# Kernel optimization log

Hardware: AMD Instinct MI355X
Metric: run time of the kernel (lower is better)

## Reference

```python
import jax, jax.numpy as jnp
import numpy as np

N, B, CIN = 2048, 16, 1
M = 4096
COUT = 64
R = 128


def setup_inputs() -> dict:
    key = jax.random.key(0)
    k1, k2, k3, k4, k5 = jax.random.split(key, 5)
    return {
        "context_in": jax.random.normal(k1, (N, B, CIN), dtype=jnp.float32),
        "context_out": jax.random.normal(k2, (N, B, COUT), dtype=jnp.float32),
        "target_in": jax.random.normal(k3, (M, B, CIN), dtype=jnp.float32),
        "lengthscale": jnp.ones((1,), dtype=jnp.float32),
        "W": jax.random.normal(k4, (R, COUT + 1), dtype=jnp.float32),
        "b": jax.random.normal(k5, (R,), dtype=jnp.float32),
    }


def reference(context_in, context_out, target_in, lengthscale, W, b):
    # context_in: (N,B,Cin), context_out: (N,B,Cout), target_in: (M,B,Cin)
    n, batch, _ = context_in.shape
    # density channel prepended -> (N,B,Cout+1)
    dens = jnp.ones((n, batch, 1), dtype=context_in.dtype)
    co = jnp.concatenate([dens, context_out], axis=-1)
    ci = jnp.transpose(context_in, (1, 0, 2))   # (B,N,Cin)
    ti = jnp.transpose(target_in, (1, 0, 2))    # (B,M,Cin)
    # squared pairwise distances (B,N,M)
    d2 = (jnp.sum(ci * ci, -1)[:, :, None]
          + jnp.sum(ti * ti, -1)[:, None, :]
          - 2.0 * jnp.einsum('bnd,bmd->bnm', ci, ti))
    d2 = jnp.maximum(d2, 0.0)
    # RBF kernel: exp(-0.5 * d2 / lengthscale^2)
    K = jnp.exp(-0.5 * d2 / (lengthscale[0] ** 2))  # (B,N,M)
    # weighted sum over context points: (B,M,Cout+1)
    out = jnp.einsum('nbc,bnm->bmc', co, K)
    # density normalization of non-density channels
    out = jnp.concatenate([out[..., :1], out[..., 1:] / (out[..., :1] + 1e-8)], axis=-1)
    # linear projection (Cout+1 -> R)
    out = out @ W.T + b
    return jnp.transpose(out, (1, 0, 2))  # (M,B,R)
```

## Files before the change

### kernel.cpp

```cpp
#include <hip/hip_runtime.h>
#include <hip/hip_bf16.h>


#define N_CTX 2048
#define BATCH 16
#define M_TGT 4096
#define COUT  64
#define RDIM  128

#define WS_CO_BYTES (N_CTX * BATCH * COUT * 2)
#define WS_SX_OFF   WS_CO_BYTES
#define WS_WT_OFF   (WS_SX_OFF + N_CTX * BATCH * 4)

#define SSCALE 0.8493222f

typedef __attribute__((ext_vector_type(8)))  short        bf16x8;
typedef __attribute__((ext_vector_type(4)))  float        floatx4;
typedef __attribute__((ext_vector_type(4)))  unsigned int uint4v;

#if __has_builtin(__builtin_amdgcn_exp2f)
#define EXP2F __builtin_amdgcn_exp2f
#else
#define EXP2F exp2f
#endif

static __device__ __forceinline__ unsigned int pack_bf16(float lo, float hi) {
    __hip_bfloat162 h = __float22bfloat162_rn(make_float2(lo, hi));
    return *reinterpret_cast<unsigned int*>(&h);
}
static __device__ __forceinline__ unsigned short f2bf(float f) {
    __hip_bfloat16 h = __float2bfloat16(f);
    return *reinterpret_cast<unsigned short*>(&h);
}

__global__ __launch_bounds__(256)
void convdeepset_prep(const float* __restrict__ ci, const float* __restrict__ co,
                      const float* __restrict__ ls, const float* __restrict__ W,
                      unsigned char* __restrict__ ws)
{
    unsigned short* cow = (unsigned short*)ws;
    float*          sx  = (float*)(ws + WS_SX_OFF);
    unsigned short* wt  = (unsigned short*)(ws + WS_WT_OFF);
    const int blk = blockIdx.x, tid = threadIdx.x;

    if (blk < 1024) {
        const int g    = blk * 4 + (tid >> 6);
        const int bb   = g & 15;
        const int nblk = g >> 4;
        const int c    = tid & 63;
        const float* rp = co + ((size_t)nblk * 8 * BATCH + bb) * COUT + c;
        unsigned int u[4];
#pragma unroll
        for (int j = 0; j < 4; ++j) {
            const float f0 = rp[(size_t)(2 * j)     * BATCH * COUT];
            const float f1 = rp[(size_t)(2 * j + 1) * BATCH * COUT];
            u[j] = pack_bf16(f0, f1);
        }
        *(uint4v*)&cow[(size_t)bb * 131072 + nblk * 512 + c * 8] = *(uint4v*)u;
    } else if (blk < 1152) {
        const int f = (blk - 1024) * 256 + tid;
        const int n = f & 2047, bb = f >> 11;
        const float s = SSCALE / ls[0];
        sx[bb * 2048 + n] = s * ci[(size_t)n * BATCH + bb];
    } else {
        for (int f = tid; f < 8192; f += 256) {
            const int cp = f & 7, r = (f >> 3) & 127, ch = f >> 10;
            wt[ch * 1024 + r * 8 + cp] = f2bf(W[r * 65 + 1 + ch * 8 + cp]);
        }
    }
}

__global__ __launch_bounds__(256)
void convdeepset_main(const float* __restrict__ ti, const float* __restrict__ ls,
                      const float* __restrict__ W,  const float* __restrict__ bias,
                      const unsigned char* __restrict__ ws, float* __restrict__ out)
{
    __shared__ float sxt[N_CTX];
    __shared__ unsigned short slab[2][8192];
    __shared__ unsigned short vstage[4][2][1024];
    __shared__ float w0l[RDIM], biasl[RDIM];

    const int tid  = threadIdx.x;
    const int lane = tid & 63;
    const int wv   = tid >> 6;
    const int g2   = lane >> 4;
    const int l15  = lane & 15;

    const int xcd = blockIdx.x & 7;
    const int i   = blockIdx.x >> 3;
    const int b   = xcd * 2 + (i & 1);
    const int mt  = i >> 1;
    const int m0  = mt * 128 + wv * 32;

    const float4* sxg = (const float4*)(ws + WS_SX_OFF) + b * (N_CTX / 4);
    ((float4*)sxt)[tid]       = sxg[tid];
    ((float4*)sxt)[tid + 256] = sxg[tid + 256];
    if (tid < RDIM) { w0l[tid] = W[tid * 65]; biasl[tid] = bias[tid]; }

    const float s   = SSCALE / ls[0];
    const float sy0 = s * ti[(size_t)(m0 + l15) * BATCH + b];
    const float sy1 = s * ti[(size_t)(m0 + 16 + l15) * BATCH + b];

    const unsigned short* cowb = (const unsigned short*)ws + (size_t)b * 131072;

    typedef const __attribute__((address_space(1))) unsigned int* gp_t;
    typedef __attribute__((address_space(3))) unsigned int* lp_t;
    auto stage = [&](int period, int buf) {
        const unsigned short* gsrc = cowb + (size_t)period * 8192;
#pragma unroll
        for (int j = 0; j < 4; ++j) {
            const int ch = wv * 4 + j;
            __builtin_amdgcn_global_load_lds((gp_t)(gsrc + ch * 512 + lane * 8),
                                             (lp_t)(&slab[buf][ch * 512]),
                                             16, 0, 0);
        }
    };

    const short onebf = (short)0x3F80;
    bf16x8 ones;
#pragma unroll
    for (int j = 0; j < 8; ++j) ones[j] = onebf;

    floatx4 acc0[4], acc1[4], accd0, accd1;
#pragma unroll
    for (int q = 0; q < 4; ++q)
#pragma unroll
        for (int e = 0; e < 4; ++e) { acc0[q][e] = 0.0f; acc1[q][e] = 0.0f; }
#pragma unroll
    for (int e = 0; e < 4; ++e) { accd0[e] = 0.0f; accd1[e] = 0.0f; }

    stage(0, 0);
    __syncthreads();

    for (int p = 0; p < 16; ++p) {
        if (p + 1 < 16) stage(p + 1, (p + 1) & 1);
        const unsigned short* sb = &slab[p & 1][0];
#pragma unroll
        for (int k2 = 0; k2 < 4; ++k2) {
            const int ks = p * 4 + k2;
            const float* xp = &sxt[ks * 32 + g2 * 8];
            const float4 xa = *(const float4*)(xp);
            const float4 xb = *(const float4*)(xp + 4);
            const unsigned short* bp = sb + (k2 * 4 + g2) * 512 + l15 * 8;
            const bf16x8 c0 = *(const bf16x8*)(bp);
            const bf16x8 c1 = *(const bf16x8*)(bp + 128);
            const bf16x8 c2 = *(const bf16x8*)(bp + 256);
            const bf16x8 c3 = *(const bf16x8*)(bp + 384);
            const float xs[8] = {xa.x, xa.y, xa.z, xa.w, xb.x, xb.y, xb.z, xb.w};
            float kv0[8], kv1[8];
#pragma unroll
            for (int j = 0; j < 8; ++j) {
                float t0 = xs[j] - sy0; kv0[j] = EXP2F(-(t0 * t0));
                float t1 = xs[j] - sy1; kv1[j] = EXP2F(-(t1 * t1));
            }
            uint4v aw0, aw1;
#pragma unroll
            for (int q = 0; q < 4; ++q) {
                aw0[q] = pack_bf16(kv0[2 * q], kv0[2 * q + 1]);
                aw1[q] = pack_bf16(kv1[2 * q], kv1[2 * q + 1]);
            }
            const bf16x8 av0 = __builtin_bit_cast(bf16x8, aw0);
            const bf16x8 av1 = __builtin_bit_cast(bf16x8, aw1);
            acc0[0] = __builtin_amdgcn_mfma_f32_16x16x32_bf16(av0, c0, acc0[0], 0, 0, 0);
            acc0[1] = __builtin_amdgcn_mfma_f32_16x16x32_bf16(av0, c1, acc0[1], 0, 0, 0);
            acc0[2] = __builtin_amdgcn_mfma_f32_16x16x32_bf16(av0, c2, acc0[2], 0, 0, 0);
            acc0[3] = __builtin_amdgcn_mfma_f32_16x16x32_bf16(av0, c3, acc0[3], 0, 0, 0);
            accd0   = __builtin_amdgcn_mfma_f32_16x16x32_bf16(av0, ones, accd0, 0, 0, 0);
            acc1[0] = __builtin_amdgcn_mfma_f32_16x16x32_bf16(av1, c0, acc1[0], 0, 0, 0);
            acc1[1] = __builtin_amdgcn_mfma_f32_16x16x32_bf16(av1, c1, acc1[1], 0, 0, 0);
            acc1[2] = __builtin_amdgcn_mfma_f32_16x16x32_bf16(av1, c2, acc1[2], 0, 0, 0);
            acc1[3] = __builtin_amdgcn_mfma_f32_16x16x32_bf16(av1, c3, acc1[3], 0, 0, 0);
            accd1   = __builtin_amdgcn_mfma_f32_16x16x32_bf16(av1, ones, accd1, 0, 0, 0);
        }
        __syncthreads();
    }

    const unsigned short* wtg = (const unsigned short*)(ws + WS_WT_OFF);
#pragma unroll
    for (int tile = 0; tile < 2; ++tile) {
        const floatx4* acc  = tile ? acc1 : acc0;
        const floatx4  accd = tile ? accd1 : accd0;
        float drow[4], dinv[4];
#pragma unroll
        for (int e = 0; e < 4; ++e) {
            drow[e] = accd[e];
            dinv[e] = 1.0f / (accd[e] + 1e-8f);
        }
        unsigned short* vs = vstage[wv][tile];
#pragma unroll
        for (int reg = 0; reg < 4; ++reg) {
            const int m = (lane >> 4) * 4 + reg;
#pragma unroll
            for (int q = 0; q < 4; ++q) {
                const int c = q * 16 + l15;
                vs[(c >> 3) * 128 + m * 8 + (c & 7)] = f2bf(acc[q][reg]);
            }
        }
        floatx4 pacc[8];
#pragma unroll
        for (int rt = 0; rt < 8; ++rt)
#pragma unroll
            for (int e = 0; e < 4; ++e) pacc[rt][e] = 0.0f;
#pragma unroll
        for (int s2 = 0; s2 < 2; ++s2) {
            const int ch = s2 * 4 + g2;
            const bf16x8 avp = *(const bf16x8*)&vs[ch * 128 + l15 * 8];
#pragma unroll
            for (int rt = 0; rt < 8; ++rt) {
                const bf16x8 bvp = *(const bf16x8*)&wtg[ch * 1024 + (rt * 16 + l15) * 8];
                pacc[rt] = __builtin_amdgcn_mfma_f32_16x16x32_bf16(avp, bvp, pacc[rt], 0, 0, 0);
            }
        }
#pragma unroll
        for (int rt = 0; rt < 8; ++rt) {
            const int r = rt * 16 + l15;
            const float w0v = w0l[r];
            const float bv  = biasl[r];
#pragma unroll
            for (int reg = 0; reg < 4; ++reg) {
                const int m = (lane >> 4) * 4 + reg;
                out[((size_t)(m0 + tile * 16 + m) * BATCH + b) * RDIM + r]
                    = pacc[rt][reg] * dinv[reg] + drow[reg] * w0v + bv;
            }
        }
    }
}

extern "C" void kernel_launch(void* const* d_in, const int* in_sizes, int n_in,
                              void* d_out, int out_size, void* d_ws, size_t ws_size,
                              hipStream_t stream) {
    const float* ci   = (const float*)d_in[0];
    const float* co   = (const float*)d_in[1];
    const float* ti   = (const float*)d_in[2];
    const float* ls   = (const float*)d_in[3];
    const float* W    = (const float*)d_in[4];
    const float* bias = (const float*)d_in[5];
    float* o = (float*)d_out;
    (void)in_sizes; (void)n_in; (void)out_size; (void)ws_size;

    convdeepset_prep<<<1153, 256, 0, stream>>>(ci, co, ls, W, (unsigned char*)d_ws);
    convdeepset_main<<<512, 256, 0, stream>>>(
        ti, ls, W, bias, (const unsigned char*)d_ws, o);
}
```

Baseline: 121.9 us.

## Factor RBF exponent into FMA form and use 512-thread blocks

The exponent -(x-y)^2 is rewritten as 2xy - x^2 with the -y^2 factor applied once in the epilogue (exp(-y^2) scales both density and channel sums, so normalization cancels it). The per-element kernel cost drops from sub, mul, neg to a single FMA before exp2. Blocks are doubled to 512 threads, with each wave owning one 16-row target tile instead of two, halving accumulator registers and raising wave count. Risk: numerical range of exp2(2xy - x^2) can overflow or underflow differently than the original for large |y|, and the density output row is reconstructed by multiplication.

```diff
diff --git a/kernel.cpp b/kernel.cpp
--- a/kernel.cpp
+++ b/kernel.cpp
@@ -9,8 +9,9 @@
 #define RDIM  128
 
 #define WS_CO_BYTES (N_CTX * BATCH * COUT * 2)
-#define WS_SX_OFF   WS_CO_BYTES
-#define WS_WT_OFF   (WS_SX_OFF + N_CTX * BATCH * 4)
+#define WS_SXA_OFF  WS_CO_BYTES
+#define WS_SXB_OFF  (WS_SXA_OFF + N_CTX * BATCH * 4)
+#define WS_WT_OFF   (WS_SXB_OFF + N_CTX * BATCH * 4)
 
 #define SSCALE 0.8493222f
 
@@ -39,7 +40,8 @@
                       unsigned char* __restrict__ ws)
 {
     unsigned short* cow = (unsigned short*)ws;
-    float*          sx  = (float*)(ws + WS_SX_OFF);
+    float*          sxa = (float*)(ws + WS_SXA_OFF);
+    float*          sxb = (float*)(ws + WS_SXB_OFF);
     unsigned short* wt  = (unsigned short*)(ws + WS_WT_OFF);
     const int blk = blockIdx.x, tid = threadIdx.x;
 
@@ -61,7 +63,9 @@
         const int f = (blk - 1024) * 256 + tid;
         const int n = f & 2047, bb = f >> 11;
         const float s = SSCALE / ls[0];
-        sx[bb * 2048 + n] = s * ci[(size_t)n * BATCH + bb];
+        const float v = s * ci[(size_t)n * BATCH + bb];
+        sxa[bb * 2048 + n] = v + v;
+        sxb[bb * 2048 + n] = -v * v;
     } else {
         for (int f = tid; f < 8192; f += 256) {
             const int cp = f & 7, r = (f >> 3) & 127, ch = f >> 10;
@@ -70,15 +74,17 @@
     }
 }
 
-__global__ __launch_bounds__(256)
+__global__ __launch_bounds__(512, 4)
 void convdeepset_main(const float* __restrict__ ti, const float* __restrict__ ls,
                       const float* __restrict__ W,  const float* __restrict__ bias,
                       const unsigned char* __restrict__ ws, float* __restrict__ out)
 {
-    __shared__ float sxt[N_CTX];
+    __shared__ float sxa[N_CTX];
+    __shared__ float sxb[N_CTX];
     __shared__ unsigned short slab[2][8192];
-    __shared__ unsigned short vstage[4][2][1024];
+    __shared__ unsigned short vstage[8][1024];
     __shared__ float w0l[RDIM], biasl[RDIM];
+    __shared__ float syt[128];
 
     const int tid  = threadIdx.x;
     const int lane = tid & 63;
@@ -90,16 +96,17 @@
     const int i   = blockIdx.x >> 3;
     const int b   = xcd * 2 + (i & 1);
     const int mt  = i >> 1;
-    const int m0  = mt * 128 + wv * 32;
-
-    const float4* sxg = (const float4*)(ws + WS_SX_OFF) + b * (N_CTX / 4);
-    ((float4*)sxt)[tid]       = sxg[tid];
-    ((float4*)sxt)[tid + 256] = sxg[tid + 256];
+    const int m0  = mt * 128 + wv * 16;
+
+    const float4* sag = (const float4*)(ws + WS_SXA_OFF) + b * (N_CTX / 4);
+    const float4* sbg = (const float4*)(ws + WS_SXB_OFF) + b * (N_CTX / 4);
+    ((float4*)sxa)[tid] = sag[tid];
+    ((float4*)sxb)[tid] = sbg[tid];
     if (tid < RDIM) { w0l[tid] = W[tid * 65]; biasl[tid] = bias[tid]; }
 
-    const float s   = SSCALE / ls[0];
-    const float sy0 = s * ti[(size_t)(m0 + l15) * BATCH + b];
-    const float sy1 = s * ti[(size_t)(m0 + 16 + l15) * BATCH + b];
+    const float s  = SSCALE / ls[0];
+    const float sy = s * ti[(size_t)(m0 + l15) * BATCH + b];
+    if (g2 == 0) syt[wv * 16 + l15] = sy * sy;
 
     const unsigned short* cowb = (const unsigned short*)ws + (size_t)b * 131072;
 
@@ -108,8 +115,8 @@
     auto stage = [&](int period, int buf) {
         const unsigned short* gsrc = cowb + (size_t)period * 8192;
 #pragma unroll
-        for (int j = 0; j < 4; ++j) {
-            const int ch = wv * 4 + j;
+        for (int j = 0; j < 2; ++j) {
+            const int ch = wv * 2 + j;
             __builtin_amdgcn_global_load_lds((gp_t)(gsrc + ch * 512 + lane * 8),
                                              (lp_t)(&slab[buf][ch * 512]),
                                              16, 0, 0);
@@ -121,13 +128,13 @@
 #pragma unroll
     for (int j = 0; j < 8; ++j) ones[j] = onebf;
 
-    floatx4 acc0[4], acc1[4], accd0, accd1;
+    floatx4 acc[4], accd;
 #pragma unroll
     for (int q = 0; q < 4; ++q)
 #pragma unroll
-        for (int e = 0; e < 4; ++e) { acc0[q][e] = 0.0f; acc1[q][e] = 0.0f; }
-#pragma unroll
-    for (int e = 0; e < 4; ++e) { accd0[e] = 0.0f; accd1[e] = 0.0f; }
+        for (int e = 0; e < 4; ++e) acc[q][e] = 0.0f;
+#pragma unroll
+    for (int e = 0; e < 4; ++e) accd[e] = 0.0f;
 
     stage(0, 0);
     __syncthreads();
@@ -138,90 +145,80 @@
 #pragma unroll
         for (int k2 = 0; k2 < 4; ++k2) {
             const int ks = p * 4 + k2;
-            const float* xp = &sxt[ks * 32 + g2 * 8];
-            const float4 xa = *(const float4*)(xp);
-            const float4 xb = *(const float4*)(xp + 4);
+            const float* xap = &sxa[ks * 32 + g2 * 8];
+            const float* xbp = &sxb[ks * 32 + g2 * 8];
+            const floatx4 arg0 = (*(const floatx4*)xap)       * sy + (*(const floatx4*)xbp);
+            const floatx4 arg1 = (*(const floatx4*)(xap + 4)) * sy + (*(const floatx4*)(xbp + 4));
             const unsigned short* bp = sb + (k2 * 4 + g2) * 512 + l15 * 8;
             const bf16x8 c0 = *(const bf16x8*)(bp);
             const bf16x8 c1 = *(const bf16x8*)(bp + 128);
             const bf16x8 c2 = *(const bf16x8*)(bp + 256);
             const bf16x8 c3 = *(const bf16x8*)(bp + 384);
-            const float xs[8] = {xa.x, xa.y, xa.z, xa.w, xb.x, xb.y, xb.z, xb.w};
-            float kv0[8], kv1[8];
-#pragma unroll
-            for (int j = 0; j < 8; ++j) {
-                float t0 = xs[j] - sy0; kv0[j] = EXP2F(-(t0 * t0));
-                float t1 = xs[j] - sy1; kv1[j] = EXP2F(-(t1 * t1));
-            }
-            uint4v aw0, aw1;
-#pragma unroll
-            for (int q = 0; q < 4; ++q) {
-                aw0[q] = pack_bf16(kv0[2 * q], kv0[2 * q + 1]);
-                aw1[q] = pack_bf16(kv1[2 * q], kv1[2 * q + 1]);
-            }
-            const bf16x8 av0 = __builtin_bit_cast(bf16x8, aw0);
-            const bf16x8 av1 = __builtin_bit_cast(bf16x8, aw1);
-            acc0[0] = __builtin_amdgcn_mfma_f32_16x16x32_bf16(av0, c0, acc0[0], 0, 0, 0);
-            acc0[1] = __builtin_amdgcn_mfma_f32_16x16x32_bf16(av0, c1, acc0[1], 0, 0, 0);
-            acc0[2] = __builtin_amdgcn_mfma_f32_16x16x32_bf16(av0, c2, acc0[2], 0, 0, 0);
-            acc0[3] = __builtin_amdgcn_mfma_f32_16x16x32_bf16(av0, c3, acc0[3], 0, 0, 0);
-            accd0   = __builtin_amdgcn_mfma_f32_16x16x32_bf16(av0, ones, accd0, 0, 0, 0);
-            acc1[0] = __builtin_amdgcn_mfma_f32_16x16x32_bf16(av1, c0, acc1[0], 0, 0, 0);
-            acc1[1] = __builtin_amdgcn_mfma_f32_16x16x32_bf16(av1, c1, acc1[1], 0, 0, 0);
-            acc1[2] = __builtin_amdgcn_mfma_f32_16x16x32_bf16(av1, c2, acc1[2], 0, 0, 0);
-            acc1[3] = __builtin_amdgcn_mfma_f32_16x16x32_bf16(av1, c3, acc1[3], 0, 0, 0);
-            accd1   = __builtin_amdgcn_mfma_f32_16x16x32_bf16(av1, ones, accd1, 0, 0, 0);
+            float kv[8];
+            kv[0] = EXP2F(arg0.x); kv[1] = EXP2F(arg0.y);
+            kv[2] = EXP2F(arg0.z); kv[3] = EXP2F(arg0.w);
+            kv[4] = EXP2F(arg1.x); kv[5] = EXP2F(arg1.y);
+            kv[6] = EXP2F(arg1.z); kv[7] = EXP2F(arg1.w);
+            uint4v aw;
+#pragma unroll
+            for (int q = 0; q < 4; ++q)
+                aw[q] = pack_bf16(kv[2 * q], kv[2 * q + 1]);
+            const bf16x8 av = __builtin_bit_cast(bf16x8, aw);
+            acc[0] = __builtin_amdgcn_mfma_f32_16x16x32_bf16(av, c0, acc[0], 0, 0, 0);
+            acc[1] = __builtin_amdgcn_mfma_f32_16x16x32_bf16(av, c1, acc[1], 0, 0, 0);
+            acc[2] = __builtin_amdgcn_mfma_f32_16x16x32_bf16(av, c2, acc[2], 0, 0, 0);
+            acc[3] = __builtin_amdgcn_mfma_f32_16x16x32_bf16(av, c3, acc[3], 0, 0, 0);
+            accd   = __builtin_amdgcn_mfma_f32_16x16x32_bf16(av, ones, accd, 0, 0, 0);
         }
         __syncthreads();
     }
 
     const unsigned short* wtg = (const unsigned short*)(ws + WS_WT_OFF);
-#pragma unroll
-    for (int tile = 0; tile < 2; ++tile) {
-        const floatx4* acc  = tile ? acc1 : acc0;
-        const floatx4  accd = tile ? accd1 : accd0;
-        float drow[4], dinv[4];
-#pragma unroll
-        for (int e = 0; e < 4; ++e) {
-            drow[e] = accd[e];
-            dinv[e] = 1.0f / (accd[e] + 1e-8f);
-        }
-        unsigned short* vs = vstage[wv][tile];
+
+    float dt[4], ff[4];
+#pragma unroll
+    for (int reg = 0; reg < 4; ++reg) {
+        const int m  = (lane >> 4) * 4 + reg;
+        const float e = EXP2F(-syt[wv * 16 + m]);
+        dt[reg] = accd[reg] * e;
+        ff[reg] = e / (dt[reg] + 1e-8f);
+    }
+
+    unsigned short* vs = vstage[wv];
+#pragma unroll
+    for (int reg = 0; reg < 4; ++reg) {
+        const int m = (lane >> 4) * 4 + reg;
+#pragma unroll
+        for (int q = 0; q < 4; ++q) {
+            const int c = q * 16 + l15;
+            vs[(c >> 3) * 128 + m * 8 + (c & 7)] = f2bf(acc[q][reg]);
+        }
+    }
+    floatx4 pacc[8];
+#pragma unroll
+    for (int rt = 0; rt < 8; ++rt)
+#pragma unroll
+        for (int e = 0; e < 4; ++e) pacc[rt][e] = 0.0f;
+#pragma unroll
+    for (int s2 = 0; s2 < 2; ++s2) {
+        const int ch = s2 * 4 + g2;
+        const bf16x8 avp = *(const bf16x8*)&vs[ch * 128 + l15 * 8];
+#pragma unroll
+        for (int rt = 0; rt < 8; ++rt) {
+            const bf16x8 bvp = *(const bf16x8*)&wtg[ch * 1024 + (rt * 16 + l15) * 8];
+            pacc[rt] = __builtin_amdgcn_mfma_f32_16x16x32_bf16(avp, bvp, pacc[rt], 0, 0, 0);
+        }
+    }
+#pragma unroll
+    for (int rt = 0; rt < 8; ++rt) {
+        const int r = rt * 16 + l15;
+        const float w0v = w0l[r];
+        const float bv  = biasl[r];
 #pragma unroll
         for (int reg = 0; reg < 4; ++reg) {
             const int m = (lane >> 4) * 4 + reg;
-#pragma unroll
-            for (int q = 0; q < 4; ++q) {
-                const int c = q * 16 + l15;
-                vs[(c >> 3) * 128 + m * 8 + (c & 7)] = f2bf(acc[q][reg]);
-            }
-        }
-        floatx4 pacc[8];
-#pragma unroll
-        for (int rt = 0; rt < 8; ++rt)
-#pragma unroll
-            for (int e = 0; e < 4; ++e) pacc[rt][e] = 0.0f;
-#pragma unroll
-        for (int s2 = 0; s2 < 2; ++s2) {
-            const int ch = s2 * 4 + g2;
-            const bf16x8 avp = *(const bf16x8*)&vs[ch * 128 + l15 * 8];
-#pragma unroll
-            for (int rt = 0; rt < 8; ++rt) {
-                const bf16x8 bvp = *(const bf16x8*)&wtg[ch * 1024 + (rt * 16 + l15) * 8];
-                pacc[rt] = __builtin_amdgcn_mfma_f32_16x16x32_bf16(avp, bvp, pacc[rt], 0, 0, 0);
-            }
-        }
-#pragma unroll
-        for (int rt = 0; rt < 8; ++rt) {
-            const int r = rt * 16 + l15;
-            const float w0v = w0l[r];
-            const float bv  = biasl[r];
-#pragma unroll
-            for (int reg = 0; reg < 4; ++reg) {
-                const int m = (lane >> 4) * 4 + reg;
-                out[((size_t)(m0 + tile * 16 + m) * BATCH + b) * RDIM + r]
-                    = pacc[rt][reg] * dinv[reg] + drow[reg] * w0v + bv;
-            }
+            out[((size_t)(m0 + m) * BATCH + b) * RDIM + r]
+                = pacc[rt][reg] * ff[reg] + dt[reg] * w0v + bv;
         }
     }
 }
@@ -239,6 +236,6 @@
     (void)in_sizes; (void)n_in; (void)out_size; (void)ws_size;
 
     convdeepset_prep<<<1153, 256, 0, stream>>>(ci, co, ls, W, (unsigned char*)d_ws);
-    convdeepset_main<<<512, 256, 0, stream>>>(
+    convdeepset_main<<<512, 512, 0, stream>>>(
         ti, ls, W, bias, (const unsigned char*)d_ws, o);
 }
```

After: 115.8 us. 1.05x faster.

## Factor RBF exponent algebraically and stream context tiles directly from global into registers

Applied to the files above, without the earlier changes.

The exponent -(x-y)^2 is expanded into 2xy - x^2 - y^2, with 2x and -x^2 precomputed in the prep kernel, so the inner loop does one FMA per element before exp2. The per-target factor exp2(-y^2) is applied afterwards in the epilogue to both the density and the normalisation. The LDS double-buffered staging of context values and positions is replaced with a register double-buffer (two Slots) that loads directly from global memory, which removes the block barriers but raises register pressure and relies on cache reuse across waves. Pulling exp2(-y^2) out of the sum can underflow for targets far from the origin, which risks precision loss.

```diff
diff --git a/kernel.cpp b/kernel.cpp
--- a/kernel.cpp
+++ b/kernel.cpp
@@ -9,8 +9,9 @@
 #define RDIM  128
 
 #define WS_CO_BYTES (N_CTX * BATCH * COUT * 2)
-#define WS_SX_OFF   WS_CO_BYTES
-#define WS_WT_OFF   (WS_SX_OFF + N_CTX * BATCH * 4)
+#define WS_SXA_OFF  WS_CO_BYTES
+#define WS_SXB_OFF  (WS_SXA_OFF + N_CTX * BATCH * 4)
+#define WS_WT_OFF   (WS_SXB_OFF + N_CTX * BATCH * 4)
 
 #define SSCALE 0.8493222f
 
@@ -39,7 +40,8 @@
                       unsigned char* __restrict__ ws)
 {
     unsigned short* cow = (unsigned short*)ws;
-    float*          sx  = (float*)(ws + WS_SX_OFF);
+    float*          sxa = (float*)(ws + WS_SXA_OFF);
+    float*          sxb = (float*)(ws + WS_SXB_OFF);
     unsigned short* wt  = (unsigned short*)(ws + WS_WT_OFF);
     const int blk = blockIdx.x, tid = threadIdx.x;
 
@@ -61,7 +63,9 @@
         const int f = (blk - 1024) * 256 + tid;
         const int n = f & 2047, bb = f >> 11;
         const float s = SSCALE / ls[0];
-        sx[bb * 2048 + n] = s * ci[(size_t)n * BATCH + bb];
+        const float v = s * ci[(size_t)n * BATCH + bb];
+        sxa[bb * 2048 + n] = v + v;
+        sxb[bb * 2048 + n] = -v * v;
     } else {
         for (int f = tid; f < 8192; f += 256) {
             const int cp = f & 7, r = (f >> 3) & 127, ch = f >> 10;
@@ -69,16 +73,18 @@
         }
     }
 }
+
+struct Slot {
+    bf16x8  c0, c1, c2, c3;
+    floatx4 xa0, xa1, xb0, xb1;
+};
 
 __global__ __launch_bounds__(256)
 void convdeepset_main(const float* __restrict__ ti, const float* __restrict__ ls,
                       const float* __restrict__ W,  const float* __restrict__ bias,
                       const unsigned char* __restrict__ ws, float* __restrict__ out)
 {
-    __shared__ float sxt[N_CTX];
-    __shared__ unsigned short slab[2][8192];
     __shared__ unsigned short vstage[4][2][1024];
-    __shared__ float w0l[RDIM], biasl[RDIM];
 
     const int tid  = threadIdx.x;
     const int lane = tid & 63;
@@ -92,29 +98,13 @@
     const int mt  = i >> 1;
     const int m0  = mt * 128 + wv * 32;
 
-    const float4* sxg = (const float4*)(ws + WS_SX_OFF) + b * (N_CTX / 4);
-    ((float4*)sxt)[tid]       = sxg[tid];
-    ((float4*)sxt)[tid + 256] = sxg[tid + 256];
-    if (tid < RDIM) { w0l[tid] = W[tid * 65]; biasl[tid] = bias[tid]; }
-
     const float s   = SSCALE / ls[0];
     const float sy0 = s * ti[(size_t)(m0 + l15) * BATCH + b];
     const float sy1 = s * ti[(size_t)(m0 + 16 + l15) * BATCH + b];
 
     const unsigned short* cowb = (const unsigned short*)ws + (size_t)b * 131072;
-
-    typedef const __attribute__((address_space(1))) unsigned int* gp_t;
-    typedef __attribute__((address_space(3))) unsigned int* lp_t;
-    auto stage = [&](int period, int buf) {
-        const unsigned short* gsrc = cowb + (size_t)period * 8192;
-#pragma unroll
-        for (int j = 0; j < 4; ++j) {
-            const int ch = wv * 4 + j;
-            __builtin_amdgcn_global_load_lds((gp_t)(gsrc + ch * 512 + lane * 8),
-                                             (lp_t)(&slab[buf][ch * 512]),
-                                             16, 0, 0);
-        }
-    };
+    const float* sxa = (const float*)(ws + WS_SXA_OFF) + b * N_CTX;
+    const float* sxb = (const float*)(ws + WS_SXB_OFF) + b * N_CTX;
 
     const short onebf = (short)0x3F80;
     bf16x8 ones;
@@ -129,62 +119,79 @@
 #pragma unroll
     for (int e = 0; e < 4; ++e) { accd0[e] = 0.0f; accd1[e] = 0.0f; }
 
-    stage(0, 0);
-    __syncthreads();
-
-    for (int p = 0; p < 16; ++p) {
-        if (p + 1 < 16) stage(p + 1, (p + 1) & 1);
-        const unsigned short* sb = &slab[p & 1][0];
-#pragma unroll
-        for (int k2 = 0; k2 < 4; ++k2) {
-            const int ks = p * 4 + k2;
-            const float* xp = &sxt[ks * 32 + g2 * 8];
-            const float4 xa = *(const float4*)(xp);
-            const float4 xb = *(const float4*)(xp + 4);
-            const unsigned short* bp = sb + (k2 * 4 + g2) * 512 + l15 * 8;
-            const bf16x8 c0 = *(const bf16x8*)(bp);
-            const bf16x8 c1 = *(const bf16x8*)(bp + 128);
-            const bf16x8 c2 = *(const bf16x8*)(bp + 256);
-            const bf16x8 c3 = *(const bf16x8*)(bp + 384);
-            const float xs[8] = {xa.x, xa.y, xa.z, xa.w, xb.x, xb.y, xb.z, xb.w};
-            float kv0[8], kv1[8];
-#pragma unroll
-            for (int j = 0; j < 8; ++j) {
-                float t0 = xs[j] - sy0; kv0[j] = EXP2F(-(t0 * t0));
-                float t1 = xs[j] - sy1; kv1[j] = EXP2F(-(t1 * t1));
-            }
-            uint4v aw0, aw1;
-#pragma unroll
-            for (int q = 0; q < 4; ++q) {
-                aw0[q] = pack_bf16(kv0[2 * q], kv0[2 * q + 1]);
-                aw1[q] = pack_bf16(kv1[2 * q], kv1[2 * q + 1]);
-            }
-            const bf16x8 av0 = __builtin_bit_cast(bf16x8, aw0);
-            const bf16x8 av1 = __builtin_bit_cast(bf16x8, aw1);
-            acc0[0] = __builtin_amdgcn_mfma_f32_16x16x32_bf16(av0, c0, acc0[0], 0, 0, 0);
-            acc0[1] = __builtin_amdgcn_mfma_f32_16x16x32_bf16(av0, c1, acc0[1], 0, 0, 0);
-            acc0[2] = __builtin_amdgcn_mfma_f32_16x16x32_bf16(av0, c2, acc0[2], 0, 0, 0);
-            acc0[3] = __builtin_amdgcn_mfma_f32_16x16x32_bf16(av0, c3, acc0[3], 0, 0, 0);
-            accd0   = __builtin_amdgcn_mfma_f32_16x16x32_bf16(av0, ones, accd0, 0, 0, 0);
-            acc1[0] = __builtin_amdgcn_mfma_f32_16x16x32_bf16(av1, c0, acc1[0], 0, 0, 0);
-            acc1[1] = __builtin_amdgcn_mfma_f32_16x16x32_bf16(av1, c1, acc1[1], 0, 0, 0);
-            acc1[2] = __builtin_amdgcn_mfma_f32_16x16x32_bf16(av1, c2, acc1[2], 0, 0, 0);
-            acc1[3] = __builtin_amdgcn_mfma_f32_16x16x32_bf16(av1, c3, acc1[3], 0, 0, 0);
-            accd1   = __builtin_amdgcn_mfma_f32_16x16x32_bf16(av1, ones, accd1, 0, 0, 0);
-        }
-        __syncthreads();
+    auto loadk = [&](Slot& S, int k) {
+        const unsigned short* bp = cowb + ((k * 4 + g2) << 9) + l15 * 8;
+        S.c0 = *(const bf16x8*)(bp);
+        S.c1 = *(const bf16x8*)(bp + 128);
+        S.c2 = *(const bf16x8*)(bp + 256);
+        S.c3 = *(const bf16x8*)(bp + 384);
+        const float* ap  = sxa + k * 32 + g2 * 8;
+        const float* bpx = sxb + k * 32 + g2 * 8;
+        S.xa0 = *(const floatx4*)(ap);
+        S.xa1 = *(const floatx4*)(ap + 4);
+        S.xb0 = *(const floatx4*)(bpx);
+        S.xb1 = *(const floatx4*)(bpx + 4);
+    };
+
+    auto compute = [&](const Slot& S) {
+        const floatx4 a00 = S.xa0 * sy0 + S.xb0;
+        const floatx4 a01 = S.xa1 * sy0 + S.xb1;
+        const floatx4 a10 = S.xa0 * sy1 + S.xb0;
+        const floatx4 a11 = S.xa1 * sy1 + S.xb1;
+        float kv0[8], kv1[8];
+        kv0[0] = EXP2F(a00.x); kv0[1] = EXP2F(a00.y);
+        kv0[2] = EXP2F(a00.z); kv0[3] = EXP2F(a00.w);
+        kv0[4] = EXP2F(a01.x); kv0[5] = EXP2F(a01.y);
+        kv0[6] = EXP2F(a01.z); kv0[7] = EXP2F(a01.w);
+        kv1[0] = EXP2F(a10.x); kv1[1] = EXP2F(a10.y);
+        kv1[2] = EXP2F(a10.z); kv1[3] = EXP2F(a10.w);
+        kv1[4] = EXP2F(a11.x); kv1[5] = EXP2F(a11.y);
+        kv1[6] = EXP2F(a11.z); kv1[7] = EXP2F(a11.w);
+        uint4v aw0, aw1;
+#pragma unroll
+        for (int q = 0; q < 4; ++q) {
+            aw0[q] = pack_bf16(kv0[2 * q], kv0[2 * q + 1]);
+            aw1[q] = pack_bf16(kv1[2 * q], kv1[2 * q + 1]);
+        }
+        const bf16x8 av0 = __builtin_bit_cast(bf16x8, aw0);
+        const bf16x8 av1 = __builtin_bit_cast(bf16x8, aw1);
+        acc0[0] = __builtin_amdgcn_mfma_f32_16x16x32_bf16(av0, S.c0, acc0[0], 0, 0, 0);
+        acc0[1] = __builtin_amdgcn_mfma_f32_16x16x32_bf16(av0, S.c1, acc0[1], 0, 0, 0);
+        acc0[2] = __builtin_amdgcn_mfma_f32_16x16x32_bf16(av0, S.c2, acc0[2], 0, 0, 0);
+        acc0[3] = __builtin_amdgcn_mfma_f32_16x16x32_bf16(av0, S.c3, acc0[3], 0, 0, 0);
+        accd0   = __builtin_amdgcn_mfma_f32_16x16x32_bf16(av0, ones, accd0, 0, 0, 0);
+        acc1[0] = __builtin_amdgcn_mfma_f32_16x16x32_bf16(av1, S.c0, acc1[0], 0, 0, 0);
+        acc1[1] = __builtin_amdgcn_mfma_f32_16x16x32_bf16(av1, S.c1, acc1[1], 0, 0, 0);
+        acc1[2] = __builtin_amdgcn_mfma_f32_16x16x32_bf16(av1, S.c2, acc1[2], 0, 0, 0);
+        acc1[3] = __builtin_amdgcn_mfma_f32_16x16x32_bf16(av1, S.c3, acc1[3], 0, 0, 0);
+        accd1   = __builtin_amdgcn_mfma_f32_16x16x32_bf16(av1, ones, accd1, 0, 0, 0);
+    };
+
+    Slot A, B;
+    loadk(A, 0);
+    for (int p = 0; p < 64; p += 2) {
+        loadk(B, p + 1);
+        compute(A);
+        if (p + 2 < 64) loadk(A, p + 2);
+        compute(B);
     }
 
     const unsigned short* wtg = (const unsigned short*)(ws + WS_WT_OFF);
+    const float sy0sq = sy0 * sy0;
+    const float sy1sq = sy1 * sy1;
 #pragma unroll
     for (int tile = 0; tile < 2; ++tile) {
         const floatx4* acc  = tile ? acc1 : acc0;
         const floatx4  accd = tile ? accd1 : accd0;
-        float drow[4], dinv[4];
-#pragma unroll
-        for (int e = 0; e < 4; ++e) {
-            drow[e] = accd[e];
-            dinv[e] = 1.0f / (accd[e] + 1e-8f);
+        const float    sysq = tile ? sy1sq : sy0sq;
+        float dt[4], ff[4];
+#pragma unroll
+        for (int reg = 0; reg < 4; ++reg) {
+            const int m   = (lane >> 4) * 4 + reg;
+            const float ysq = __shfl(sysq, m, 64);
+            const float e   = EXP2F(-ysq);
+            dt[reg] = accd[reg] * e;
+            ff[reg] = e / (dt[reg] + 1e-8f);
         }
         unsigned short* vs = vstage[wv][tile];
 #pragma unroll
@@ -214,13 +221,13 @@
 #pragma unroll
         for (int rt = 0; rt < 8; ++rt) {
             const int r = rt * 16 + l15;
-            const float w0v = w0l[r];
-            const float bv  = biasl[r];
+            const float w0v = W[r * 65];
+            const float bv  = bias[r];
 #pragma unroll
             for (int reg = 0; reg < 4; ++reg) {
                 const int m = (lane >> 4) * 4 + reg;
                 out[((size_t)(m0 + tile * 16 + m) * BATCH + b) * RDIM + r]
-                    = pacc[rt][reg] * dinv[reg] + drow[reg] * w0v + bv;
+                    = pacc[rt][reg] * ff[reg] + dt[reg] * w0v + bv;
             }
         }
     }
```

Result: slower. 129.7 us (+6.4%).
